# Performance work log

Hardware: AMD Instinct MI355X
Metric: run time of the kernel (lower is better)

The kernel has to match this reference:

```python
import jax, jax.numpy as jnp
import numpy as np
import math

B, L, D = 4, 4096, 1024
D_EMB, D_HID = 3, 16


def make_pos_emb(emb_dim, seq_len):
    # Complex exponential positional embeddings (non-trainable), shape (1, seq_len, emb_dim)
    t = np.linspace(0.0, 1.0, seq_len, dtype=np.float32)[None, :, None]
    bands = (emb_dim - 1) // 2
    t_res = np.linspace(0.0, seq_len - 1, seq_len, dtype=np.float32)[None, :, None]
    w = 2.0 * math.pi * t_res / seq_len
    f = np.linspace(0.0001, max(bands - 1, 0), bands, dtype=np.float32)[None, None]
    z = np.exp(-1j * (f * w).astype(np.complex64))
    z = np.concatenate([t, z.real.astype(np.float32), z.imag.astype(np.float32)], axis=-1)
    return jnp.asarray(z)


def setup_inputs() -> dict:
    key = jax.random.key(0)
    ks = jax.random.split(key, 8)
    u = jax.random.normal(ks[0], (B, L, D), dtype=jnp.float32)
    z = make_pos_emb(D_EMB, L)  # (1, L, D_EMB)
    # filter MLP: Linear(d_emb, d_hidden) -> ReLU -> Linear(d_hidden, d_model)
    s1 = 1.0 / math.sqrt(D_EMB)
    w1 = jax.random.uniform(ks[1], (D_HID, D_EMB), jnp.float32, -s1, s1)
    b1 = jax.random.uniform(ks[2], (D_HID,), jnp.float32, -s1, s1)
    s2 = 1.0 / math.sqrt(D_HID)
    w2 = jax.random.uniform(ks[3], (D, D_HID), jnp.float32, -s2, s2)
    b2 = jax.random.uniform(ks[4], (D,), jnp.float32, -s2, s2)
    # projection: Linear(d_model, d_model)
    sp = 1.0 / math.sqrt(D)
    pw = jax.random.uniform(ks[5], (D, D), jnp.float32, -sp, sp)
    pb = jax.random.uniform(ks[6], (D,), jnp.float32, -sp, sp)
    return {"u": u, "z": z, "w1": w1, "b1": b1, "w2": w2, "b2": b2, "pw": pw, "pb": pb}


def fft_conv(u_bdl, k_dl):
    # u_bdl: (B, D, L), k_dl: (1, D, L) or (D, L)
    seqlen = u_bdl.shape[-1]
    fft_size = 2 * seqlen
    k_f = jnp.fft.rfft(k_dl, n=fft_size) / fft_size
    u_f = jnp.fft.rfft(u_bdl, n=fft_size)
    y = jnp.fft.irfft(u_f * k_f, n=fft_size, norm="forward")[..., :seqlen]
    return y


def reference(u, z, w1, b1, w2, b2, pw, pb):
    seqlen = u.shape[1]
    pe = z[:, :seqlen]  # (1, L, D_EMB)
    h = jax.nn.relu(jnp.einsum("ble,he->blh", pe, w1) + b1)
    filt = jnp.einsum("blh,dh->bld", h, w2) + b2  # (1, L, D)
    filt = jnp.transpose(filt, (0, 2, 1))  # (1, D, L)
    u_conv = fft_conv(jnp.transpose(u, (0, 2, 1)), filt)  # (B, D, L)
    u_conv = jnp.transpose(u_conv, (0, 2, 1)).astype(u.dtype)  # (B, L, D)
    u_proj = jnp.einsum("bld,od->blo", u, pw) + pb
    return u_conv * u_proj + u
```

## Files before the change

kernel.cpp:

```cpp
#include <hip/hip_runtime.h>
#include <hip/hip_bf16.h>

#define SEQL 4096
#define DCH  1024
#define BATCH 4
#define KH   4097

typedef __attribute__((ext_vector_type(2))) float cf;
__device__ __forceinline__ cf mkc(float x, float y){ cf r; r.x = x; r.y = y; return r; }
__device__ __forceinline__ cf cadd(cf a, cf b){ return a + b; }
__device__ __forceinline__ cf csub(cf a, cf b){ return a - b; }
__device__ __forceinline__ cf cmul(cf a, cf b){ return a.xx * b + mkc(-a.y, a.y) * b.yx; }
__device__ __forceinline__ cf cconjf(cf a){ return mkc(a.x, -a.y); }
__device__ __forceinline__ cf addi(cf a, cf b){ return a + mkc(-b.y, b.x); }
__device__ __forceinline__ cf subi(cf a, cf b){ return a - mkc(-b.y, b.x); }
__device__ __forceinline__ int phi(int c){ return c ^ ((c >> 4) & 15); }
__device__ __forceinline__ int drev(int i){
    return ((i>>10)&3) | (((i>>8)&3)<<2) | (((i>>6)&3)<<4)
         | (((i>>4)&3)<<6) | (((i>>2)&3)<<8) | ((i&3)<<10);
}

__device__ __forceinline__ cf W1c(int j){
    const float cs[4] = {1.f, 0.92387953f, 0.70710678f, 0.38268343f};
    const float sn[4] = {0.f, -0.38268343f, -0.70710678f, -0.92387953f};
    return mkc(cs[j], sn[j]);
}
__device__ __forceinline__ cf W2c(int j){
    const float cs[4] = {1.f, 0.70710678f, 0.f, -0.70710678f};
    const float sn[4] = {0.f, -0.70710678f, -1.f, -0.70710678f};
    return mkc(cs[j], sn[j]);
}
__device__ __forceinline__ cf W3c(int j){
    const float cs[4] = {1.f, 0.38268343f, -0.70710678f, -0.92387953f};
    const float sn[4] = {0.f, -0.92387953f, -0.70710678f, 0.38268343f};
    return mkc(cs[j], sn[j]);
}

__device__ __forceinline__ unsigned pack2bf(float a, float b){
    unsigned r;
    asm("v_cvt_pk_bf16_f32 %0, %1, %2" : "=v"(r) : "v"(a), "v"(b));
    return r;
}
__device__ __forceinline__ float bflo(unsigned u){ return __uint_as_float(u << 16); }
__device__ __forceinline__ float bfhi(unsigned u){ return __uint_as_float(u & 0xffff0000u); }

__device__ __forceinline__ void gload16(const void* g, void* l){
    __builtin_amdgcn_global_load_lds((const __attribute__((address_space(1))) void*)g,
                                     (__attribute__((address_space(3))) void*)l, 16, 0, 0);
}

__global__ __launch_bounds__(256) void twiddle_init(cf* __restrict__ tw4, cf* __restrict__ tw8){
    int i = blockIdx.x*256 + threadIdx.x;
    const double TWO_PI = 6.283185307179586476925286766559;
    double a4 = -TWO_PI * (double)i / 4096.0;
    double a8 = -TWO_PI * (double)i / 8192.0;
    tw4[i] = mkc((float)cos(a4), (float)sin(a4));
    tw8[i] = mkc((float)cos(a8), (float)sin(a8));
}

__global__ __launch_bounds__(256) void mlp_kernel(
        const float* __restrict__ z, const float* __restrict__ w1,
        const float* __restrict__ b1, float* __restrict__ h) {
    int l = blockIdx.x * blockDim.x + threadIdx.x;
    if (l >= SEQL) return;
    float pe0 = z[l * 3 + 0], pe1 = z[l * 3 + 1], pe2 = z[l * 3 + 2];
#pragma unroll
    for (int j = 0; j < 16; ++j) {
        float v = pe0 * w1[j * 3 + 0] + pe1 * w1[j * 3 + 1] + pe2 * w1[j * 3 + 2] + b1[j];
        h[l * 16 + j] = v > 0.f ? v : 0.f;
    }
}

__global__ __launch_bounds__(256) void transpose_kernel(
        const float* __restrict__ u, unsigned* __restrict__ utb,
        unsigned short* __restrict__ ub) {
    __shared__ float tile[32][33];
    int b = blockIdx.z;
    int l0 = blockIdx.x * 32;
    int d0 = blockIdx.y * 32;
    int tx = threadIdx.x, ty = threadIdx.y;
    const float* up = u + (size_t)b * SEQL * DCH;
    unsigned short* ubp = ub ? ub + (size_t)b * SEQL * DCH : (unsigned short*)0;
#pragma unroll
    for (int i = 0; i < 32; i += 8) {
        size_t idx = (size_t)(l0 + ty + i) * DCH + d0 + tx;
        float v = up[idx];
        tile[ty + i][tx] = v;
        if (ub) ubp[idx] = (unsigned short)pack2bf(v, v);
    }
    __syncthreads();
    unsigned* utp = utb + (size_t)b * DCH * (SEQL / 2);
    int t  = ty * 32 + tx;
    int dl = t >> 4;
    int lp = t & 15;
#pragma unroll
    for (int p = 0; p < 2; ++p) {
        int dd = dl + p * 16;
        unsigned v = pack2bf(tile[2 * lp][dd], tile[2 * lp + 1][dd]);
        utp[(size_t)(d0 + dd) * (SEQL / 2) + (l0 >> 1) + lp] = v;
    }
}

__global__ __launch_bounds__(256) void pw2bf_kernel(
        const float* __restrict__ pw, unsigned short* __restrict__ pwb) {
    int t = blockIdx.x * 256 + threadIdx.x;
    float4 a = *(const float4*)&pw[(size_t)t * 8];
    float4 b = *(const float4*)&pw[(size_t)t * 8 + 4];
    uint4 o;
    o.x = pack2bf(a.x, a.y); o.y = pack2bf(a.z, a.w);
    o.z = pack2bf(b.x, b.y); o.w = pack2bf(b.z, b.w);
    *(uint4*)&pwb[(size_t)t * 8] = o;
}

__device__ void dif_mid_and_chunk(cf* lds, const cf* __restrict__ tw){
    const int tid = threadIdx.x;
#pragma unroll
    for (int p = 1; p < 4; ++p) {
        const int lm = 10 - 2*p;
        const int m  = 1 << lm;
        const int step = 1024 >> lm;
#pragma unroll
        for (int it = 0; it < 4; ++it) {
            int j = tid + (it << 8);
            int k = j & (m-1);
            int g = j >> lm;
            int i0 = (g << (lm+2)) + k;
            cf x0 = lds[phi(i0)];
            cf x1 = lds[phi(i0+m)];
            cf x2 = lds[phi(i0+2*m)];
            cf x3 = lds[phi(i0+3*m)];
            cf b0 = cadd(x0,x2), b1 = csub(x0,x2);
            cf b2 = cadd(x1,x3), b3 = csub(x1,x3);
            cf u0 = cadd(b0,b2);
            cf u2 = csub(b0,b2);
            cf u1 = subi(b1,b3);
            cf u3 = addi(b1,b3);
            int t1 = k*step;
            lds[phi(i0)]     = u0;
            lds[phi(i0+m)]   = cmul(u1, tw[t1]);
            lds[phi(i0+2*m)] = cmul(u2, tw[2*t1]);
            lds[phi(i0+3*m)] = cmul(u3, tw[3*t1]);
        }
        __syncthreads();
    }
    {
        const int b0 = tid << 4;
        const int xr = tid & 15;
        cf v[16];
#pragma unroll
        for (int j=0;j<16;++j) v[j] = lds[b0 + (j ^ xr)];
#pragma unroll
        for (int j=0;j<4;++j){
            cf x0=v[j], x1=v[j+4], x2=v[j+8], x3=v[j+12];
            cf b0v=cadd(x0,x2), b1=csub(x0,x2), b2=cadd(x1,x3), b3=csub(x1,x3);
            cf u0=cadd(b0v,b2), u2=csub(b0v,b2), u1=subi(b1,b3), u3=addi(b1,b3);
            v[j]    = u0;
            v[j+4]  = cmul(u1, W1c(j));
            v[j+8]  = cmul(u2, W2c(j));
            v[j+12] = cmul(u3, W3c(j));
        }
#pragma unroll
        for (int c=0;c<4;++c){
            cf x0=v[4*c], x1=v[4*c+1], x2=v[4*c+2], x3=v[4*c+3];
            cf b0v=cadd(x0,x2), b1=csub(x0,x2), b2=cadd(x1,x3), b3=csub(x1,x3);
            v[4*c]   = cadd(b0v,b2);
            v[4*c+1] = subi(b1,b3);
            v[4*c+2] = csub(b0v,b2);
            v[4*c+3] = addi(b1,b3);
        }
#pragma unroll
        for (int j=0;j<16;++j) lds[b0 + (j ^ xr)] = v[j];
        __syncthreads();
    }
}

__device__ void dit_chunk_and_mid(cf* lds, const cf* __restrict__ tw){
    const int tid = threadIdx.x;
    {
        const int b0 = tid << 4;
        const int xr = tid & 15;
        cf v[16];
#pragma unroll
        for (int j=0;j<16;++j) v[j] = lds[b0 + (j ^ xr)];
#pragma unroll
        for (int c=0;c<4;++c){
            cf a0=v[4*c], a1=v[4*c+1], a2=v[4*c+2], a3=v[4*c+3];
            cf b0v=cadd(a0,a2), b1=csub(a0,a2), b2=cadd(a1,a3), b3=csub(a1,a3);
            v[4*c]   = cadd(b0v,b2);
            v[4*c+1] = addi(b1,b3);
            v[4*c+2] = csub(b0v,b2);
            v[4*c+3] = subi(b1,b3);
        }
#pragma unroll
        for (int j=0;j<4;++j){
            cf a0=v[j];
            cf a1=cmul(v[j+4],  cconjf(W1c(j)));
            cf a2=cmul(v[j+8],  cconjf(W2c(j)));
            cf a3=cmul(v[j+12], cconjf(W3c(j)));
            cf b0v=cadd(a0,a2), b1=csub(a0,a2), b2=cadd(a1,a3), b3=csub(a1,a3);
            v[j]    = cadd(b0v,b2);
            v[j+4]  = addi(b1,b3);
            v[j+8]  = csub(b0v,b2);
            v[j+12] = subi(b1,b3);
        }
#pragma unroll
        for (int j=0;j<16;++j) lds[b0 + (j ^ xr)] = v[j];
        __syncthreads();
    }
#pragma unroll
    for (int p = 0; p < 3; ++p) {
        const int lm = 4 + 2*p;
        const int m  = 1 << lm;
        const int step = 1024 >> lm;
#pragma unroll
        for (int it = 0; it < 4; ++it) {
            int j = tid + (it << 8);
            int k = j & (m-1);
            int g = j >> lm;
            int i0 = (g << (lm+2)) + k;
            int t1 = k*step;
            cf a0 = lds[phi(i0)];
            cf a1 = cmul(lds[phi(i0+m)],   cconjf(tw[t1]));
            cf a2 = cmul(lds[phi(i0+2*m)], cconjf(tw[2*t1]));
            cf a3 = cmul(lds[phi(i0+3*m)], cconjf(tw[3*t1]));
            cf b0=cadd(a0,a2), b1=csub(a0,a2), b2=cadd(a1,a3), b3=csub(a1,a3);
            lds[phi(i0)]     = cadd(b0,b2);
            lds[phi(i0+m)]   = addi(b1,b3);
            lds[phi(i0+2*m)] = csub(b0,b2);
            lds[phi(i0+3*m)] = subi(b1,b3);
        }
        __syncthreads();
    }
}

__global__ __launch_bounds__(256) void filt_fft_kernel(
        const float* __restrict__ h, const float* __restrict__ w2,
        const float* __restrict__ b2, const cf* __restrict__ tw4,
        const cf* __restrict__ tw8, cf* __restrict__ kf) {
    __shared__ cf lds[4096];
    const int d = blockIdx.x;
    const int tid = threadIdx.x;
    float wv[16];
#pragma unroll
    for (int j = 0; j < 16; ++j) wv[j] = w2[d * 16 + j];
    const float bb = b2[d];
#pragma unroll
    for (int it = 0; it < 4; ++it) {
        int j = tid + (it << 8);
        const float* h0 = h + (size_t)(2*j) * 16;
        const float* h1 = h + (size_t)(2*(j+1024)) * 16;
        float f0 = bb, f1 = bb, f2 = bb, f3 = bb;
#pragma unroll
        for (int i = 0; i < 16; ++i) {
            f0 += h0[i] * wv[i];  f1 += h0[16+i] * wv[i];
            f2 += h1[i] * wv[i];  f3 += h1[16+i] * wv[i];
        }
        cf x0 = mkc(f0, f1), x1 = mkc(f2, f3);
        cf u0 = cadd(x0,x1);
        cf u2 = csub(x0,x1);
        cf u1 = subi(x0,x1);
        cf u3 = addi(x0,x1);
        lds[phi(j)]      = u0;
        lds[phi(j+1024)] = cmul(u1, tw4[j]);
        lds[phi(j+2048)] = cmul(u2, tw4[2*j]);
        lds[phi(j+3072)] = cmul(u3, tw4[3*j]);
    }
    __syncthreads();
    dif_mid_and_chunk(lds, tw4);
    const float s = 1.f / 8192.f;
    cf* Hrow = kf + (size_t)d * KH;
    const int lane  = tid & 63;
    const int kbase = ((lane & 31) << 6) | ((lane >> 5) << 5) | ((tid >> 6) << 3);
#pragma unroll
    for (int it = 0; it < 8; ++it) {
        int k = kbase + it;
        if (k == 0) {
            cf c0 = lds[0];
            Hrow[0]    = mkc((c0.x + c0.y) * s, 0.f);
            Hrow[4096] = mkc((c0.x - c0.y) * s, 0.f);
            cf c2 = lds[phi(drev(2048))];
            Hrow[2048] = mkc(c2.x * s, -c2.y * s);
        } else {
            int kk = 4096 - k;
            cf ck  = lds[phi(drev(k))];
            cf ckk = lds[phi(drev(kk))];
            cf cc = cconjf(ckk);
            cf E  = (ck + cc) * 0.5f;
            cf Dd = csub(ck, cc);
            cf O  = mkc(Dd.y, -Dd.x) * 0.5f;
            cf wvv = tw8[k];
            cf Xk  = cadd(E, cmul(wvv, O));
            cf wp  = mkc(-wvv.x, wvv.y);
            cf Xkk = cadd(cconjf(E), cmul(wp, cconjf(O)));
            Hrow[k]  = Xk * s;
            Hrow[kk] = Xkk * s;
        }
    }
}

__global__ __launch_bounds__(256) void conv_kernel(
        unsigned* __restrict__ utyb, const cf* __restrict__ tw4,
        const cf* __restrict__ tw8, const cf* __restrict__ kf) {
    __shared__ cf lds[4096];
    const int row = blockIdx.x;
    const int d = row & (DCH - 1);
    const int tid = threadIdx.x;
    unsigned* rp = utyb + (size_t)row * (SEQL / 2);
#pragma unroll
    for (int it = 0; it < 4; ++it) {
        int j = tid + (it << 8);
        unsigned q0 = rp[j], q1 = rp[j + 1024];
        cf x0 = mkc(bflo(q0), bfhi(q0));
        cf x1 = mkc(bflo(q1), bfhi(q1));
        cf u0 = cadd(x0,x1);
        cf u2 = csub(x0,x1);
        cf u1 = subi(x0,x1);
        cf u3 = addi(x0,x1);
        lds[phi(j)]      = u0;
        lds[phi(j+1024)] = cmul(u1, tw4[j]);
        lds[phi(j+2048)] = cmul(u2, tw4[2*j]);
        lds[phi(j+3072)] = cmul(u3, tw4[3*j]);
    }
    __syncthreads();
    dif_mid_and_chunk(lds, tw4);
    const cf* Hrow = kf + (size_t)d * KH;
    {
        const int lane  = tid & 63;
        const int kbase = ((lane & 31) << 6) | ((lane >> 5) << 5) | ((tid >> 6) << 3);
#pragma unroll
        for (int it = 0; it < 8; ++it) {
            int k = kbase + it;
            if (k == 0) {
                cf c0 = lds[0];
                float X0 = c0.x + c0.y, X4 = c0.x - c0.y;
                cf H0 = Hrow[0], H4 = Hrow[4096];
                cf Y0 = H0 * X0;
                cf Y4 = H4 * X4;
                cf S  = cadd(Y0, Y4), Dd = csub(Y0, Y4);
                lds[0] = addi(S, Dd);
                int s2 = phi(drev(2048));
                cf c2 = lds[s2];
                cf Y2 = cmul(cconjf(c2), Hrow[2048]);
                lds[s2] = mkc(2.f * Y2.x, -2.f * Y2.y);
            } else {
                int kk = 4096 - k;
                int sk = phi(drev(k)), skk = phi(drev(kk));
                cf ck = lds[sk], ckk = lds[skk];
                cf cc = cconjf(ckk);
                cf E  = (ck + cc) * 0.5f;
                cf Dd = csub(ck, cc);
                cf O  = mkc(Dd.y, -Dd.x) * 0.5f;
                cf wv = tw8[k];
                cf Xk  = cadd(E, cmul(wv, O));
                cf wp  = mkc(-wv.x, wv.y);
                cf Xkk = cadd(cconjf(E), cmul(wp, cconjf(O)));
                cf Yk  = cmul(Xk,  Hrow[k]);
                cf Ykk = cmul(Xkk, Hrow[kk]);
                cf cy = cconjf(Ykk);
                cf S  = cadd(Yk, cy), D2 = csub(Yk, cy);
                cf Zk = addi(S, cmul(cconjf(wv), D2));
                cf cy2 = cconjf(Yk);
                cf S2  = cadd(Ykk, cy2), D3 = csub(Ykk, cy2);
                cf Zkk = subi(S2, cmul(wv, D3));
                lds[sk] = Zk; lds[skk] = Zkk;
            }
        }
    }
    __syncthreads();
    dit_chunk_and_mid(lds, tw4);
#pragma unroll
    for (int it = 0; it < 4; ++it) {
        int j = tid + (it << 8);
        cf a0 = lds[phi(j)];
        cf a1 = cmul(lds[phi(j+1024)], cconjf(tw4[j]));
        cf a2 = cmul(lds[phi(j+2048)], cconjf(tw4[2*j]));
        cf a3 = cmul(lds[phi(j+3072)], cconjf(tw4[3*j]));
        cf b0 = cadd(a0,a2), b1 = csub(a0,a2);
        cf b2 = cadd(a1,a3), b3 = csub(a1,a3);
        cf o0 = cadd(b0,b2);
        cf o1 = addi(b1,b3);
        rp[j]        = pack2bf(o0.x, o0.y);
        rp[j + 1024] = pack2bf(o1.x, o1.y);
    }
}

typedef __attribute__((ext_vector_type(8))) short short8;
typedef __attribute__((ext_vector_type(4))) float f32x4;

__global__ __launch_bounds__(512, 2) void gemm_mfma_v3(
        const unsigned short* __restrict__ ub, const unsigned short* __restrict__ pwb,
        const float* __restrict__ pb, const unsigned short* __restrict__ yb,
        float* __restrict__ out) {
    __shared__ char lds_raw[147456];
    float (*ysc)[132] = (float(*)[132])lds_raw;

    const int tid  = threadIdx.x;
    const int lane = tid & 63;
    const int wid  = tid >> 6;
    const int wr   = wid >> 1;
    const int wc   = wid & 1;
    const int m0   = blockIdx.x * 256;
    const int n0   = blockIdx.y * 128;

    f32x4 acc[4][4] = {};

#pragma unroll
    for (int tt = 0; tt < 2; ++tt) {
#pragma unroll
        for (int un = 0; un < 3; ++un) {
            const unsigned short* gs = (un == 2) ? pwb : ub;
            int growb = (un == 2) ? n0 : (m0 + un * 128);
#pragma unroll
            for (int j = 0; j < 2; ++j) {
                int rr = j * 64 + (tid >> 3);
                int ss = (tid & 7) ^ ((tid >> 3) & 7);
                gload16(gs + (size_t)(growb + rr) * 1024 + tt * 64 + ss * 8,
                        lds_raw + tt * 49152 + un * 16384 + rr * 128 + (tid & 7) * 16);
            }
        }
    }
    asm volatile("s_waitcnt vmcnt(6)" ::: "memory");
    __builtin_amdgcn_sched_barrier(0);
    __builtin_amdgcn_s_barrier();

    for (int t = 0; t < 16; ++t) {
        const int Ab  = (t % 3) * 49152;
        const int Bb  = Ab + 32768;
        const int sbB = ((t + 2) % 3) * 49152;
        const int kt2 = (t + 2) * 64;
#pragma unroll
        for (int q = 0; q < 4; ++q) {
            const int qr = q >> 1, qc = q & 1;
            short8 af[2][2], bfr[2][2];
#pragma unroll
            for (int f = 0; f < 2; ++f) {
                int arow = wr * 64 + qr * 32 + f * 16 + (lane & 15);
                int brow = wc * 64 + qc * 32 + f * 16 + (lane & 15);
#pragma unroll
                for (int kh = 0; kh < 2; ++kh) {
                    int ks = (lane >> 4) + 4 * kh;
                    af[f][kh]  = *(short8*)(lds_raw + Ab + arow * 128 + (ks ^ (arow & 7)) * 16);
                    bfr[f][kh] = *(short8*)(lds_raw + Bb + brow * 128 + (ks ^ (brow & 7)) * 16);
                }
            }
            if (q < 3 && t < 14) {
                const unsigned short* gs = (q == 2) ? pwb : ub;
                int growb = (q == 2) ? n0 : (m0 + q * 128);
#pragma unroll
                for (int j = 0; j < 2; ++j) {
                    int rr = j * 64 + (tid >> 3);
                    int ss = (tid & 7) ^ ((tid >> 3) & 7);
                    gload16(gs + (size_t)(growb + rr) * 1024 + kt2 + ss * 8,
                            lds_raw + sbB + q * 16384 + rr * 128 + (tid & 7) * 16);
                }
            }
            __builtin_amdgcn_s_barrier();
            asm volatile("s_waitcnt lgkmcnt(0)" ::: "memory");
            __builtin_amdgcn_sched_barrier(0);
            __builtin_amdgcn_s_setprio(1);
#pragma unroll
            for (int fa = 0; fa < 2; ++fa)
#pragma unroll
                for (int fb = 0; fb < 2; ++fb)
#pragma unroll
                    for (int kh = 0; kh < 2; ++kh)
                        acc[qr * 2 + fa][qc * 2 + fb] = __builtin_amdgcn_mfma_f32_16x16x32_bf16(
                            af[fa][kh], bfr[fb][kh], acc[qr * 2 + fa][qc * 2 + fb], 0, 0, 0);
            __builtin_amdgcn_s_setprio(0);
            if (q == 3) {
                if (t < 14)       asm volatile("s_waitcnt vmcnt(6)" ::: "memory");
                else if (t == 14) asm volatile("s_waitcnt vmcnt(0)" ::: "memory");
                __builtin_amdgcn_sched_barrier(0);
            }
            __builtin_amdgcn_s_barrier();
        }
    }

    __syncthreads();
    const int b  = m0 >> 12;
    const int l0 = m0 & (SEQL - 1);
    float pbv[4];
#pragma unroll
    for (int nf = 0; nf < 4; ++nf)
        pbv[nf] = pb[n0 + wc * 64 + nf * 16 + (lane & 15)];

    for (int c = 0; c < 2; ++c) {
        __syncthreads();
        {
            int dn = tid >> 2;
            int lq = tid & 3;
            const uint4* uptr = (const uint4*)(yb + (((size_t)(b * DCH + n0 + dn)) << 12) + l0 + c * 128);
#pragma unroll
            for (int jj = 0; jj < 4; ++jj) {
                uint4 w4 = uptr[lq * 4 + jj];
                int lb = (lq * 4 + jj) * 8;
                ysc[lb+0][dn] = bflo(w4.x); ysc[lb+1][dn] = bfhi(w4.x);
                ysc[lb+2][dn] = bflo(w4.y); ysc[lb+3][dn] = bfhi(w4.y);
                ysc[lb+4][dn] = bflo(w4.z); ysc[lb+5][dn] = bfhi(w4.z);
                ysc[lb+6][dn] = bflo(w4.w); ysc[lb+7][dn] = bfhi(w4.w);
            }
        }
        __syncthreads();
        if ((wr >> 1) == c) {
#pragma unroll
            for (int mf = 0; mf < 4; ++mf)
#pragma unroll
                for (int i = 0; i < 4; ++i) {
                    int lrow = (wr & 1) * 64 + mf * 16 + (lane >> 4) * 4 + i;
                    int m = m0 + c * 128 + lrow;
#pragma unroll
                    for (int nf = 0; nf < 4; ++nf) {
                        int nl = wc * 64 + nf * 16 + (lane & 15);
                        int n = n0 + nl;
                        float proj = acc[mf][nf][i] + pbv[nf];
                        float ures = __uint_as_float((unsigned)ub[(size_t)m * DCH + n] << 16);
                        out[(size_t)m * DCH + n] = ysc[lrow][nl] * proj + ures;
                    }
                }
        }
    }
}

__global__ __launch_bounds__(256, 3) void gemm_mfma_fb(
        const float* __restrict__ u, const float* __restrict__ pw,
        const float* __restrict__ pb, const unsigned short* __restrict__ yb,
        float* __restrict__ out) {
    __shared__ char lds_raw[34816];
    float (*ysc)[132] = (float(*)[132])lds_raw;
    const int tid  = threadIdx.x;
    const int lane = tid & 63;
    const int wid  = tid >> 6;
    const int wr   = wid >> 1;
    const int wc   = wid & 1;
    const int m0   = blockIdx.x * 128;
    const int n0   = blockIdx.y * 128;
    f32x4 acc[4][4] = {};
    float4 ra[4], rb[4];
    int s_row[4], s_f4[4];
#pragma unroll
    for (int j = 0; j < 4; ++j) {
        int idx = j * 256 + tid;
        s_row[j] = idx >> 3;
        s_f4[j]  = idx & 7;
    }
#define LOADT(kt)                                                                     \
    {                                                                                 \
        _Pragma("unroll")                                                             \
        for (int j = 0; j < 4; ++j) {                                                 \
            ra[j] = *(const float4*)&u [(size_t)(m0 + s_row[j]) * DCH + (kt) + s_f4[j] * 4]; \
            rb[j] = *(const float4*)&pw[(size_t)(n0 + s_row[j]) * DCH + (kt) + s_f4[j] * 4]; \
        }                                                                             \
    }
#define WRITET(base)                                                                  \
    {                                                                                 \
        _Pragma("unroll")                                                             \
        for (int j = 0; j < 4; ++j) {                                                 \
            int off = (base) + ((s_row[j] * 64 + s_f4[j] * 8) ^ ((s_row[j] & 3) << 4)); \
            uint2 pa, pbv2;                                                           \
            pa.x   = pack2bf(ra[j].x, ra[j].y);  pa.y   = pack2bf(ra[j].z, ra[j].w);  \
            pbv2.x = pack2bf(rb[j].x, rb[j].y);  pbv2.y = pack2bf(rb[j].z, rb[j].w);  \
            *(uint2*)(lds_raw + off)        = pa;                                     \
            *(uint2*)(lds_raw + off + 8192) = pbv2;                                   \
        }                                                                             \
    }
    LOADT(0);
    WRITET(0);
    LOADT(32);
    __syncthreads();
    for (int t = 0; t < 32; ++t) {
        const int cur = (t & 1) << 14;
        short8 af[4], bfr[4];
#pragma unroll
        for (int f = 0; f < 4; ++f) {
            int rowA = wr * 64 + f * 16 + (lane & 15);
            int rowB = wc * 64 + f * 16 + (lane & 15);
            int offA = cur + ((rowA * 64 + ((lane >> 4) * 16)) ^ ((rowA & 3) << 4));
            int offB = cur + 8192 + ((rowB * 64 + ((lane >> 4) * 16)) ^ ((rowB & 3) << 4));
            af[f]  = *(short8*)(lds_raw + offA);
            bfr[f] = *(short8*)(lds_raw + offB);
        }
        if (t < 31) WRITET(cur ^ 16384);
        if (t < 30) LOADT((t + 2) * 32);
#pragma unroll
        for (int mf = 0; mf < 4; ++mf)
#pragma unroll
            for (int nf = 0; nf < 4; ++nf)
                acc[mf][nf] = __builtin_amdgcn_mfma_f32_16x16x32_bf16(
                    af[mf], bfr[nf], acc[mf][nf], 0, 0, 0);
        __syncthreads();
    }
    const int b  = m0 >> 12;
    const int l0 = m0 & (SEQL - 1);
    float pbv[4];
#pragma unroll
    for (int nf = 0; nf < 4; ++nf)
        pbv[nf] = pb[n0 + wc * 64 + nf * 16 + (lane & 15)];
    for (int c = 0; c < 2; ++c) {
        __syncthreads();
#pragma unroll
        for (int j = 0; j < 4; ++j) {
            int idx = j * 256 + tid;
            int dn  = idx >> 3;
            int lg  = idx & 7;
            uint4 w4 = *(const uint4*)&yb[(((size_t)(b * DCH + n0 + dn)) << 12) + l0 + c * 64 + lg * 8];
            int lb = lg * 8;
            ysc[lb+0][dn] = bflo(w4.x); ysc[lb+1][dn] = bfhi(w4.x);
            ysc[lb+2][dn] = bflo(w4.y); ysc[lb+3][dn] = bfhi(w4.y);
            ysc[lb+4][dn] = bflo(w4.z); ysc[lb+5][dn] = bfhi(w4.z);
            ysc[lb+6][dn] = bflo(w4.w); ysc[lb+7][dn] = bfhi(w4.w);
        }
        __syncthreads();
        if (wr == c) {
#pragma unroll
            for (int mf = 0; mf < 4; ++mf)
#pragma unroll
                for (int i = 0; i < 4; ++i) {
                    int lrow = mf * 16 + (lane >> 4) * 4 + i;
                    int m = m0 + c * 64 + lrow;
#pragma unroll
                    for (int nf = 0; nf < 4; ++nf) {
                        int nl = wc * 64 + nf * 16 + (lane & 15);
                        int n = n0 + nl;
                        float proj = acc[mf][nf][i] + pbv[nf];
                        out[(size_t)m * DCH + n] = ysc[lrow][nl] * proj + u[(size_t)m * DCH + n];
                    }
                }
        }
    }
#undef LOADT
#undef WRITET
}

extern "C" void kernel_launch(void* const* d_in, const int* in_sizes, int n_in,
                              void* d_out, int out_size, void* d_ws, size_t ws_size,
                              hipStream_t stream) {
    const float* u  = (const float*)d_in[0];
    const float* z  = (const float*)d_in[1];
    const float* w1 = (const float*)d_in[2];
    const float* b1 = (const float*)d_in[3];
    const float* w2 = (const float*)d_in[4];
    const float* b2 = (const float*)d_in[5];
    const float* pw = (const float*)d_in[6];
    const float* pb = (const float*)d_in[7];
    float* out = (float*)d_out;

    float*    h    = (float*)d_ws;
    unsigned* utyb = (unsigned*)((char*)d_ws + 262144);
    cf* kf = (cf*)d_out;

    const size_t ub_off  = 262144 + (size_t)BATCH * DCH * (SEQL / 2) * sizeof(unsigned);
    const size_t pwb_off = ub_off + (size_t)BATCH * SEQL * DCH * sizeof(unsigned short);
    const size_t tw_off  = pwb_off + (size_t)DCH * DCH * sizeof(unsigned short);
    const size_t need    = tw_off + 2 * 4096 * sizeof(cf);
    const bool   big     = ws_size >= need;

    cf* tw4 = big ? (cf*)((char*)d_ws + tw_off) : (cf*)((char*)d_out + (40u << 20));
    cf* tw8 = tw4 + 4096;
    unsigned short* ub  = big ? (unsigned short*)((char*)d_ws + ub_off)  : (unsigned short*)0;
    unsigned short* pwb = big ? (unsigned short*)((char*)d_ws + pwb_off) : (unsigned short*)0;

    twiddle_init<<<dim3(16), dim3(256), 0, stream>>>(tw4, tw8);
    mlp_kernel<<<dim3(16), dim3(256), 0, stream>>>(z, w1, b1, h);
    transpose_kernel<<<dim3(SEQL / 32, DCH / 32, BATCH), dim3(32, 8), 0, stream>>>(u, utyb, ub);
    if (big) pw2bf_kernel<<<dim3(512), dim3(256), 0, stream>>>(pw, pwb);
    filt_fft_kernel<<<dim3(DCH), dim3(256), 0, stream>>>(h, w2, b2, tw4, tw8, kf);
    conv_kernel<<<dim3(BATCH * DCH), dim3(256), 0, stream>>>(utyb, tw4, tw8, kf);
    if (big)
        gemm_mfma_v3<<<dim3(64, 8), dim3(512), 0, stream>>>(ub, pwb, pb, (const unsigned short*)utyb, out);
    else
        gemm_mfma_fb<<<dim3(128, 8), dim3(256), 0, stream>>>(u, pw, pb, (const unsigned short*)utyb, out);
}
```

Before: 263.2 us.

## Repartition FFT middle stages per wavefront to drop block barriers

After the first radix-4 stage, each wavefront now owns one contiguous 1024-point sub-FFT for the three middle radix-4 stages and the 16-point chunk stage. The block-wide __syncthreads between those stages become an inline s_waitcnt lgkmcnt(0) fence, so only intra-wave LDS ordering is enforced. The forward DIF and inverse DIT paths get the same change, with explicit barriers kept only at the boundaries. This relies on wave-lockstep execution and in-order LDS completion within a wave, and it changes the LDS access patterns, which could affect bank conflicts.

After: 266.8 us. Within noise of the previous version (+1.4%).

```diff
diff --git a/kernel.cpp b/kernel.cpp
--- a/kernel.cpp
+++ b/kernel.cpp
@@ -19,6 +19,7 @@
     return ((i>>10)&3) | (((i>>8)&3)<<2) | (((i>>6)&3)<<4)
          | (((i>>4)&3)<<6) | (((i>>2)&3)<<8) | ((i&3)<<10);
 }
+__device__ __forceinline__ void lds_fence(){ asm volatile("s_waitcnt lgkmcnt(0)" ::: "memory"); }
 
 __device__ __forceinline__ cf W1c(int j){
     const float cs[4] = {1.f, 0.92387953f, 0.70710678f, 0.38268343f};
@@ -112,37 +113,59 @@
     *(uint4*)&pwb[(size_t)t * 8] = o;
 }
 
-__device__ void dif_mid_and_chunk(cf* lds, const cf* __restrict__ tw){
-    const int tid = threadIdx.x;
-#pragma unroll
-    for (int p = 1; p < 4; ++p) {
-        const int lm = 10 - 2*p;
-        const int m  = 1 << lm;
-        const int step = 1024 >> lm;
-#pragma unroll
-        for (int it = 0; it < 4; ++it) {
-            int j = tid + (it << 8);
-            int k = j & (m-1);
-            int g = j >> lm;
-            int i0 = (g << (lm+2)) + k;
-            cf x0 = lds[phi(i0)];
-            cf x1 = lds[phi(i0+m)];
-            cf x2 = lds[phi(i0+2*m)];
-            cf x3 = lds[phi(i0+3*m)];
-            cf b0 = cadd(x0,x2), b1 = csub(x0,x2);
-            cf b2 = cadd(x1,x3), b3 = csub(x1,x3);
-            cf u0 = cadd(b0,b2);
-            cf u2 = csub(b0,b2);
-            cf u1 = subi(b1,b3);
-            cf u3 = addi(b1,b3);
-            int t1 = k*step;
-            lds[phi(i0)]     = u0;
-            lds[phi(i0+m)]   = cmul(u1, tw[t1]);
-            lds[phi(i0+2*m)] = cmul(u2, tw[2*t1]);
-            lds[phi(i0+3*m)] = cmul(u3, tw[3*t1]);
-        }
-        __syncthreads();
-    }
+__device__ void dif_wavelocal(cf* lds, const cf* __restrict__ tw){
+    const int tid  = threadIdx.x;
+    const int lane = tid & 63;
+    const int wid  = tid >> 6;
+#pragma unroll
+    for (int it = 0; it < 4; ++it) {
+        int k  = (it << 6) + lane;
+        int i0 = (wid << 10) + k;
+        cf x0 = lds[phi(i0)];
+        cf x1 = lds[phi(i0+256)];
+        cf x2 = lds[phi(i0+512)];
+        cf x3 = lds[phi(i0+768)];
+        cf b0 = cadd(x0,x2), b1 = csub(x0,x2);
+        cf b2 = cadd(x1,x3), b3 = csub(x1,x3);
+        lds[phi(i0)]     = cadd(b0,b2);
+        lds[phi(i0+256)] = cmul(subi(b1,b3), tw[4*k]);
+        lds[phi(i0+512)] = cmul(csub(b0,b2), tw[8*k]);
+        lds[phi(i0+768)] = cmul(addi(b1,b3), tw[12*k]);
+    }
+    lds_fence();
+#pragma unroll
+    for (int it = 0; it < 4; ++it) {
+        int g  = (wid << 2) + it;
+        int i0 = (g << 8) + lane;
+        cf x0 = lds[phi(i0)];
+        cf x1 = lds[phi(i0+64)];
+        cf x2 = lds[phi(i0+128)];
+        cf x3 = lds[phi(i0+192)];
+        cf b0 = cadd(x0,x2), b1 = csub(x0,x2);
+        cf b2 = cadd(x1,x3), b3 = csub(x1,x3);
+        lds[phi(i0)]     = cadd(b0,b2);
+        lds[phi(i0+64)]  = cmul(subi(b1,b3), tw[16*lane]);
+        lds[phi(i0+128)] = cmul(csub(b0,b2), tw[32*lane]);
+        lds[phi(i0+192)] = cmul(addi(b1,b3), tw[48*lane]);
+    }
+    lds_fence();
+#pragma unroll
+    for (int it = 0; it < 4; ++it) {
+        int k  = lane & 15;
+        int g  = (wid << 4) + (it << 2) + (lane >> 4);
+        int i0 = (g << 6) + k;
+        cf x0 = lds[phi(i0)];
+        cf x1 = lds[phi(i0+16)];
+        cf x2 = lds[phi(i0+32)];
+        cf x3 = lds[phi(i0+48)];
+        cf b0 = cadd(x0,x2), b1 = csub(x0,x2);
+        cf b2 = cadd(x1,x3), b3 = csub(x1,x3);
+        lds[phi(i0)]    = cadd(b0,b2);
+        lds[phi(i0+16)] = cmul(subi(b1,b3), tw[64*k]);
+        lds[phi(i0+32)] = cmul(csub(b0,b2), tw[128*k]);
+        lds[phi(i0+48)] = cmul(addi(b1,b3), tw[192*k]);
+    }
+    lds_fence();
     {
         const int b0 = tid << 4;
         const int xr = tid & 15;
@@ -170,12 +193,13 @@
         }
 #pragma unroll
         for (int j=0;j<16;++j) lds[b0 + (j ^ xr)] = v[j];
-        __syncthreads();
-    }
-}
-
-__device__ void dit_chunk_and_mid(cf* lds, const cf* __restrict__ tw){
-    const int tid = threadIdx.x;
+    }
+}
+
+__device__ void dit_wavelocal(cf* lds, const cf* __restrict__ tw){
+    const int tid  = threadIdx.x;
+    const int lane = tid & 63;
+    const int wid  = tid >> 6;
     {
         const int b0 = tid << 4;
         const int xr = tid & 15;
@@ -205,31 +229,55 @@
         }
 #pragma unroll
         for (int j=0;j<16;++j) lds[b0 + (j ^ xr)] = v[j];
-        __syncthreads();
-    }
-#pragma unroll
-    for (int p = 0; p < 3; ++p) {
-        const int lm = 4 + 2*p;
-        const int m  = 1 << lm;
-        const int step = 1024 >> lm;
-#pragma unroll
-        for (int it = 0; it < 4; ++it) {
-            int j = tid + (it << 8);
-            int k = j & (m-1);
-            int g = j >> lm;
-            int i0 = (g << (lm+2)) + k;
-            int t1 = k*step;
-            cf a0 = lds[phi(i0)];
-            cf a1 = cmul(lds[phi(i0+m)],   cconjf(tw[t1]));
-            cf a2 = cmul(lds[phi(i0+2*m)], cconjf(tw[2*t1]));
-            cf a3 = cmul(lds[phi(i0+3*m)], cconjf(tw[3*t1]));
-            cf b0=cadd(a0,a2), b1=csub(a0,a2), b2=cadd(a1,a3), b3=csub(a1,a3);
-            lds[phi(i0)]     = cadd(b0,b2);
-            lds[phi(i0+m)]   = addi(b1,b3);
-            lds[phi(i0+2*m)] = csub(b0,b2);
-            lds[phi(i0+3*m)] = subi(b1,b3);
-        }
-        __syncthreads();
+    }
+    lds_fence();
+#pragma unroll
+    for (int it = 0; it < 4; ++it) {
+        int k  = lane & 15;
+        int g  = (wid << 4) + (it << 2) + (lane >> 4);
+        int i0 = (g << 6) + k;
+        cf a0 = lds[phi(i0)];
+        cf a1 = cmul(lds[phi(i0+16)], cconjf(tw[64*k]));
+        cf a2 = cmul(lds[phi(i0+32)], cconjf(tw[128*k]));
+        cf a3 = cmul(lds[phi(i0+48)], cconjf(tw[192*k]));
+        cf b0 = cadd(a0,a2), b1 = csub(a0,a2);
+        cf b2 = cadd(a1,a3), b3 = csub(a1,a3);
+        lds[phi(i0)]    = cadd(b0,b2);
+        lds[phi(i0+16)] = addi(b1,b3);
+        lds[phi(i0+32)] = csub(b0,b2);
+        lds[phi(i0+48)] = subi(b1,b3);
+    }
+    lds_fence();
+#pragma unroll
+    for (int it = 0; it < 4; ++it) {
+        int g  = (wid << 2) + it;
+        int i0 = (g << 8) + lane;
+        cf a0 = lds[phi(i0)];
+        cf a1 = cmul(lds[phi(i0+64)],  cconjf(tw[16*lane]));
+        cf a2 = cmul(lds[phi(i0+128)], cconjf(tw[32*lane]));
+        cf a3 = cmul(lds[phi(i0+192)], cconjf(tw[48*lane]));
+        cf b0 = cadd(a0,a2), b1 = csub(a0,a2);
+        cf b2 = cadd(a1,a3), b3 = csub(a1,a3);
+        lds[phi(i0)]     = cadd(b0,b2);
+        lds[phi(i0+64)]  = addi(b1,b3);
+        lds[phi(i0+128)] = csub(b0,b2);
+        lds[phi(i0+192)] = subi(b1,b3);
+    }
+    lds_fence();
+#pragma unroll
+    for (int it = 0; it < 4; ++it) {
+        int k  = (it << 6) + lane;
+        int i0 = (wid << 10) + k;
+        cf a0 = lds[phi(i0)];
+        cf a1 = cmul(lds[phi(i0+256)], cconjf(tw[4*k]));
+        cf a2 = cmul(lds[phi(i0+512)], cconjf(tw[8*k]));
+        cf a3 = cmul(lds[phi(i0+768)], cconjf(tw[12*k]));
+        cf b0 = cadd(a0,a2), b1 = csub(a0,a2);
+        cf b2 = cadd(a1,a3), b3 = csub(a1,a3);
+        lds[phi(i0)]     = cadd(b0,b2);
+        lds[phi(i0+256)] = addi(b1,b3);
+        lds[phi(i0+512)] = csub(b0,b2);
+        lds[phi(i0+768)] = subi(b1,b3);
     }
 }
 
@@ -266,7 +314,8 @@
         lds[phi(j+3072)] = cmul(u3, tw4[3*j]);
     }
     __syncthreads();
-    dif_mid_and_chunk(lds, tw4);
+    dif_wavelocal(lds, tw4);
+    __syncthreads();
     const float s = 1.f / 8192.f;
     cf* Hrow = kf + (size_t)d * KH;
     const int lane  = tid & 63;
@@ -322,7 +371,8 @@
         lds[phi(j+3072)] = cmul(u3, tw4[3*j]);
     }
     __syncthreads();
-    dif_mid_and_chunk(lds, tw4);
+    dif_wavelocal(lds, tw4);
+    __syncthreads();
     const cf* Hrow = kf + (size_t)d * KH;
     {
         const int lane  = tid & 63;
@@ -367,7 +417,8 @@
         }
     }
     __syncthreads();
-    dit_chunk_and_mid(lds, tw4);
+    dit_wavelocal(lds, tw4);
+    __syncthreads();
 #pragma unroll
     for (int it = 0; it < 4; ++it) {
         int j = tid + (it << 8);
```

## Fold real-FFT split and merge into precomputed filter coefficients P, P2, Q

Applied to the files above, without the earlier changes.

Folds the real-FFT post-processing (split into even/odd with tw8), the filter multiply, and the inverse pre-processing into three precomputed per-channel complex coefficient arrays P, P2 and Q. The conv kernel then applies Zk = P·ck + Q·conj(ckk) directly, removing the twiddle loads and most of the complex arithmetic in its frequency-domain loop. Bit-reversed, swizzled LDS indices are precomputed into a lookup table. The small prep kernels (twiddle, MLP, pw-to-bf16) are merged into one launch. In exchange, the conv kernel reads three coefficient rows instead of one filter row, which adds global traffic, and more scratch space in the output buffer is used.

Result: no change. 259.1 us (-1.6%).

```diff
diff --git a/kernel.cpp b/kernel.cpp
--- a/kernel.cpp
+++ b/kernel.cpp
@@ -4,7 +4,6 @@
 #define SEQL 4096
 #define DCH  1024
 #define BATCH 4
-#define KH   4097
 
 typedef __attribute__((ext_vector_type(2))) float cf;
 __device__ __forceinline__ cf mkc(float x, float y){ cf r; r.x = x; r.y = y; return r; }
@@ -49,25 +48,40 @@
                                      (__attribute__((address_space(3))) void*)l, 16, 0, 0);
 }
 
-__global__ __launch_bounds__(256) void twiddle_init(cf* __restrict__ tw4, cf* __restrict__ tw8){
-    int i = blockIdx.x*256 + threadIdx.x;
-    const double TWO_PI = 6.283185307179586476925286766559;
-    double a4 = -TWO_PI * (double)i / 4096.0;
-    double a8 = -TWO_PI * (double)i / 8192.0;
-    tw4[i] = mkc((float)cos(a4), (float)sin(a4));
-    tw8[i] = mkc((float)cos(a8), (float)sin(a8));
-}
-
-__global__ __launch_bounds__(256) void mlp_kernel(
+__global__ __launch_bounds__(256) void prep_kernel(
+        cf* __restrict__ tw4, cf* __restrict__ tw8, unsigned* __restrict__ idxt,
         const float* __restrict__ z, const float* __restrict__ w1,
-        const float* __restrict__ b1, float* __restrict__ h) {
-    int l = blockIdx.x * blockDim.x + threadIdx.x;
-    if (l >= SEQL) return;
-    float pe0 = z[l * 3 + 0], pe1 = z[l * 3 + 1], pe2 = z[l * 3 + 2];
-#pragma unroll
-    for (int j = 0; j < 16; ++j) {
-        float v = pe0 * w1[j * 3 + 0] + pe1 * w1[j * 3 + 1] + pe2 * w1[j * 3 + 2] + b1[j];
-        h[l * 16 + j] = v > 0.f ? v : 0.f;
+        const float* __restrict__ b1, float* __restrict__ h,
+        const float* __restrict__ pw, unsigned short* __restrict__ pwb) {
+    const int blk = blockIdx.x;
+    if (blk < 16) {
+        int i = blk * 256 + threadIdx.x;
+        const double TWO_PI = 6.283185307179586476925286766559;
+        double a4 = -TWO_PI * (double)i / 4096.0;
+        double a8 = -TWO_PI * (double)i / 8192.0;
+        tw4[i] = mkc((float)cos(a4), (float)sin(a4));
+        tw8[i] = mkc((float)cos(a8), (float)sin(a8));
+    } else if (blk < 32) {
+        int l = (blk - 16) * 256 + threadIdx.x;
+        float pe0 = z[l * 3 + 0], pe1 = z[l * 3 + 1], pe2 = z[l * 3 + 2];
+#pragma unroll
+        for (int j = 0; j < 16; ++j) {
+            float v = pe0 * w1[j * 3 + 0] + pe1 * w1[j * 3 + 1] + pe2 * w1[j * 3 + 2] + b1[j];
+            h[l * 16 + j] = v > 0.f ? v : 0.f;
+        }
+    } else if (blk < 40) {
+        int k = (blk - 32) * 256 + threadIdx.x;
+        unsigned sk  = (unsigned)phi(drev(k));
+        unsigned skk = (unsigned)phi(drev(4096 - k));
+        idxt[k] = sk | (skk << 16);
+    } else if (pwb) {
+        int t = (blk - 40) * 256 + threadIdx.x;
+        float4 a = *(const float4*)&pw[(size_t)t * 8];
+        float4 b = *(const float4*)&pw[(size_t)t * 8 + 4];
+        uint4 o;
+        o.x = pack2bf(a.x, a.y); o.y = pack2bf(a.z, a.w);
+        o.z = pack2bf(b.x, b.y); o.w = pack2bf(b.z, b.w);
+        *(uint4*)&pwb[(size_t)t * 8] = o;
     }
 }
 
@@ -99,17 +113,6 @@
         unsigned v = pack2bf(tile[2 * lp][dd], tile[2 * lp + 1][dd]);
         utp[(size_t)(d0 + dd) * (SEQL / 2) + (l0 >> 1) + lp] = v;
     }
-}
-
-__global__ __launch_bounds__(256) void pw2bf_kernel(
-        const float* __restrict__ pw, unsigned short* __restrict__ pwb) {
-    int t = blockIdx.x * 256 + threadIdx.x;
-    float4 a = *(const float4*)&pw[(size_t)t * 8];
-    float4 b = *(const float4*)&pw[(size_t)t * 8 + 4];
-    uint4 o;
-    o.x = pack2bf(a.x, a.y); o.y = pack2bf(a.z, a.w);
-    o.z = pack2bf(b.x, b.y); o.w = pack2bf(b.z, b.w);
-    *(uint4*)&pwb[(size_t)t * 8] = o;
 }
 
 __device__ void dif_mid_and_chunk(cf* lds, const cf* __restrict__ tw){
@@ -236,7 +239,8 @@
 __global__ __launch_bounds__(256) void filt_fft_kernel(
         const float* __restrict__ h, const float* __restrict__ w2,
         const float* __restrict__ b2, const cf* __restrict__ tw4,
-        const cf* __restrict__ tw8, cf* __restrict__ kf) {
+        const cf* __restrict__ tw8, cf* __restrict__ kfP,
+        cf* __restrict__ kfP2, cf* __restrict__ kfQ) {
     __shared__ cf lds[4096];
     const int d = blockIdx.x;
     const int tid = threadIdx.x;
@@ -268,7 +272,9 @@
     __syncthreads();
     dif_mid_and_chunk(lds, tw4);
     const float s = 1.f / 8192.f;
-    cf* Hrow = kf + (size_t)d * KH;
+    cf* Prow  = kfP  + (size_t)d * 2048;
+    cf* P2row = kfP2 + (size_t)d * 2048;
+    cf* Qrow  = kfQ  + (size_t)d * 2048;
     const int lane  = tid & 63;
     const int kbase = ((lane & 31) << 6) | ((lane >> 5) << 5) | ((tid >> 6) << 3);
 #pragma unroll
@@ -276,10 +282,12 @@
         int k = kbase + it;
         if (k == 0) {
             cf c0 = lds[0];
-            Hrow[0]    = mkc((c0.x + c0.y) * s, 0.f);
-            Hrow[4096] = mkc((c0.x - c0.y) * s, 0.f);
-            cf c2 = lds[phi(drev(2048))];
-            Hrow[2048] = mkc(c2.x * s, -c2.y * s);
+            float H0 = (c0.x + c0.y) * s;
+            float H4 = (c0.x - c0.y) * s;
+            Prow[0]  = mkc(H0 + H4, H0 - H4);
+            P2row[0] = mkc(H0 - H4, H0 + H4);
+            cf c2 = lds[2];
+            Qrow[0] = mkc(2.f * s * c2.x, 2.f * s * c2.y);
         } else {
             int kk = 4096 - k;
             cf ck  = lds[phi(drev(k))];
@@ -292,15 +300,24 @@
             cf Xk  = cadd(E, cmul(wvv, O));
             cf wp  = mkc(-wvv.x, wvv.y);
             cf Xkk = cadd(cconjf(E), cmul(wp, cconjf(O)));
-            Hrow[k]  = Xk * s;
-            Hrow[kk] = Xkk * s;
+            cf Hk  = Xk * s;
+            cf Hkk = Xkk * s;
+            float a = 1.f + wvv.y;
+            float b = 1.f - wvv.y;
+            cf Hkb = cconjf(Hkk);
+            cf Hkc = cconjf(Hk);
+            Prow[k]  = Hk * a + Hkb * b;
+            P2row[k] = Hkk * a + Hkc * b;
+            cf Qd = csub(Hk, Hkb);
+            Qrow[k] = mkc(-Qd.y, Qd.x) * wvv.x;
         }
     }
 }
 
 __global__ __launch_bounds__(256) void conv_kernel(
         unsigned* __restrict__ utyb, const cf* __restrict__ tw4,
-        const cf* __restrict__ tw8, const cf* __restrict__ kf) {
+        const unsigned* __restrict__ idxt, const cf* __restrict__ kfP,
+        const cf* __restrict__ kfP2, const cf* __restrict__ kfQ) {
     __shared__ cf lds[4096];
     const int row = blockIdx.x;
     const int d = row & (DCH - 1);
@@ -323,7 +340,9 @@
     }
     __syncthreads();
     dif_mid_and_chunk(lds, tw4);
-    const cf* Hrow = kf + (size_t)d * KH;
+    const cf* Prow  = kfP  + (size_t)d * 2048;
+    const cf* P2row = kfP2 + (size_t)d * 2048;
+    const cf* Qrow  = kfQ  + (size_t)d * 2048;
     {
         const int lane  = tid & 63;
         const int kbase = ((lane & 31) << 6) | ((lane >> 5) << 5) | ((tid >> 6) << 3);
@@ -331,37 +350,19 @@
         for (int it = 0; it < 8; ++it) {
             int k = kbase + it;
             if (k == 0) {
+                cf P0 = Prow[0], C0 = P2row[0], Q0 = Qrow[0];
                 cf c0 = lds[0];
-                float X0 = c0.x + c0.y, X4 = c0.x - c0.y;
-                cf H0 = Hrow[0], H4 = Hrow[4096];
-                cf Y0 = H0 * X0;
-                cf Y4 = H4 * X4;
-                cf S  = cadd(Y0, Y4), Dd = csub(Y0, Y4);
-                lds[0] = addi(S, Dd);
-                int s2 = phi(drev(2048));
-                cf c2 = lds[s2];
-                cf Y2 = cmul(cconjf(c2), Hrow[2048]);
-                lds[s2] = mkc(2.f * Y2.x, -2.f * Y2.y);
+                lds[0] = P0 * c0.x + C0 * c0.y;
+                cf c2 = lds[2];
+                lds[2] = cmul(Q0, c2);
             } else {
-                int kk = 4096 - k;
-                int sk = phi(drev(k)), skk = phi(drev(kk));
+                unsigned iv = idxt[k];
+                int sk  = iv & 0xffff;
+                int skk = iv >> 16;
                 cf ck = lds[sk], ckk = lds[skk];
-                cf cc = cconjf(ckk);
-                cf E  = (ck + cc) * 0.5f;
-                cf Dd = csub(ck, cc);
-                cf O  = mkc(Dd.y, -Dd.x) * 0.5f;
-                cf wv = tw8[k];
-                cf Xk  = cadd(E, cmul(wv, O));
-                cf wp  = mkc(-wv.x, wv.y);
-                cf Xkk = cadd(cconjf(E), cmul(wp, cconjf(O)));
-                cf Yk  = cmul(Xk,  Hrow[k]);
-                cf Ykk = cmul(Xkk, Hrow[kk]);
-                cf cy = cconjf(Ykk);
-                cf S  = cadd(Yk, cy), D2 = csub(Yk, cy);
-                cf Zk = addi(S, cmul(cconjf(wv), D2));
-                cf cy2 = cconjf(Yk);
-                cf S2  = cadd(Ykk, cy2), D3 = csub(Ykk, cy2);
-                cf Zkk = subi(S2, cmul(wv, D3));
+                cf Pv = Prow[k], P2v = P2row[k], Qv = Qrow[k];
+                cf Zk  = cadd(cmul(Pv, ck),  cmul(Qv, cconjf(ckk)));
+                cf Zkk = csub(cmul(P2v, ckk), cmul(cconjf(Qv), cconjf(ck)));
                 lds[sk] = Zk; lds[skk] = Zkk;
             }
         }
@@ -646,25 +647,32 @@
 
     float*    h    = (float*)d_ws;
     unsigned* utyb = (unsigned*)((char*)d_ws + 262144);
-    cf* kf = (cf*)d_out;
+
+    cf* kfP  = (cf*)d_out;
+    cf* kfP2 = (cf*)((char*)d_out + (16u << 20));
+    cf* kfQ  = (cf*)((char*)d_out + (32u << 20));
 
     const size_t ub_off  = 262144 + (size_t)BATCH * DCH * (SEQL / 2) * sizeof(unsigned);
     const size_t pwb_off = ub_off + (size_t)BATCH * SEQL * DCH * sizeof(unsigned short);
     const size_t tw_off  = pwb_off + (size_t)DCH * DCH * sizeof(unsigned short);
-    const size_t need    = tw_off + 2 * 4096 * sizeof(cf);
+    const size_t need    = tw_off + 2 * 4096 * sizeof(cf) + 2048 * sizeof(unsigned);
     const bool   big     = ws_size >= need;
 
-    cf* tw4 = big ? (cf*)((char*)d_ws + tw_off) : (cf*)((char*)d_out + (40u << 20));
+    cf* tw4; unsigned* idxt;
+    if (big) {
+        tw4  = (cf*)((char*)d_ws + tw_off);
+    } else {
+        tw4  = (cf*)((char*)d_out + (56u << 20));
+    }
     cf* tw8 = tw4 + 4096;
+    idxt = (unsigned*)(tw8 + 4096);
     unsigned short* ub  = big ? (unsigned short*)((char*)d_ws + ub_off)  : (unsigned short*)0;
     unsigned short* pwb = big ? (unsigned short*)((char*)d_ws + pwb_off) : (unsigned short*)0;
 
-    twiddle_init<<<dim3(16), dim3(256), 0, stream>>>(tw4, tw8);
-    mlp_kernel<<<dim3(16), dim3(256), 0, stream>>>(z, w1, b1, h);
+    prep_kernel<<<dim3(big ? 552 : 40), dim3(256), 0, stream>>>(tw4, tw8, idxt, z, w1, b1, h, pw, pwb);
     transpose_kernel<<<dim3(SEQL / 32, DCH / 32, BATCH), dim3(32, 8), 0, stream>>>(u, utyb, ub);
-    if (big) pw2bf_kernel<<<dim3(512), dim3(256), 0, stream>>>(pw, pwb);
-    filt_fft_kernel<<<dim3(DCH), dim3(256), 0, stream>>>(h, w2, b2, tw4, tw8, kf);
-    conv_kernel<<<dim3(BATCH * DCH), dim3(256), 0, stream>>>(utyb, tw4, tw8, kf);
+    filt_fft_kernel<<<dim3(DCH), dim3(256), 0, stream>>>(h, w2, b2, tw4, tw8, kfP, kfP2, kfQ);
+    conv_kernel<<<dim3(BATCH * DCH), dim3(256), 0, stream>>>(utyb, tw4, idxt, kfP, kfP2, kfQ);
     if (big)
         gemm_mfma_v3<<<dim3(64, 8), dim3(512), 0, stream>>>(ub, pwb, pb, (const unsigned short*)utyb, out);
     else
```
